# Performance work log

Hardware: AMD Instinct MI355X
Metric: run time of the kernel (lower is better)

## Reference

```python
import jax, jax.numpy as jnp
import numpy as np

B, T = 2, 5            # num_frames MUST equal 5 (Embedding(5, channel) pos table)
C, CTX_C, DH = 384, 128, 64   # channel, context_channel, dim_head (lucidrains default, heads=1)
HW = [(80, 80), (40, 40), (20, 20), (10, 10)]
NS = 4
SCALE = DH ** -0.5


def _xavier(k, shape):
    fan_out, fan_in = shape[-2], shape[-1]
    lim = (6.0 / (fan_in + fan_out)) ** 0.5
    return jax.random.uniform(k, shape, jnp.float32, -lim, lim)


def setup_inputs() -> dict:
    key = jax.random.key(0)
    ks = iter(jax.random.split(key, 40))
    inp = {}
    for i, (h, w) in enumerate(HW):
        inp[f"fmap{i}"] = jax.random.normal(next(ks), (B * T, C, h, w), jnp.float32)
        inp[f"pos{i}"] = jax.random.normal(next(ks), (B, T, C, h, w), jnp.float32)
        inp[f"audio{i}"] = jax.random.normal(next(ks), (B * T, CTX_C), jnp.float32)
    inp["ctx_proj_w"] = _xavier(next(ks), (NS, C, CTX_C))
    inp["ctx_proj_b"] = jnp.zeros((NS, C), jnp.float32)
    inp["pos_emb"] = jax.random.normal(next(ks), (NS, 5, C), jnp.float32)  # Embedding(5, channel) per stage
    inp["qk_w"] = _xavier(next(ks), (NS, DH, C))
    inp["ctx_qk_w"] = _xavier(next(ks), (NS, DH, C))
    inp["v_w"] = _xavier(next(ks), (NS, DH, C))
    inp["ctx_v_w"] = _xavier(next(ks), (NS, DH, C))
    inp["out_w"] = _xavier(next(ks), (NS, C, DH))
    inp["out_b"] = jnp.zeros((NS, C), jnp.float32)
    inp["ctx_out_w"] = _xavier(next(ks), (NS, C, DH))
    inp["ctx_out_b"] = jnp.zeros((NS, C), jnp.float32)
    inp["batch_size"] = B
    inp["num_frames"] = T
    return inp


def _stage(x, pos, audio, Wp, bp, pe, Wqk, Wcqk, Wv, Wcv, Wo, bo, Wco, bco, batch_size):
    bt, c, h, w = x.shape
    # audio projection 128 -> 384
    a = audio @ Wp.T + bp                                  # (bt, C)
    # 'hw' reshape: tokens = H*W per (batch*frame)
    xf = x.reshape(bt, c, h * w).transpose(0, 2, 1)        # (bt, hw, C)
    vp = pos.reshape(bt, c, h * w).transpose(0, 2, 1)      # (bt, hw, C)
    ctx = a[:, None, :]                                    # (bt, 1, C)
    cp = jnp.tile(pe, (batch_size, 1))[:, None, :]         # (bt, 1, C); bt == 5*batch_size
    # bidirectional cross-attention (heads=1), pos added to QK inputs only
    qk = (xf + vp) @ Wqk.T                                 # (bt, hw, DH)
    v = xf @ Wv.T                                          # (bt, hw, DH)
    cqk = (ctx + cp) @ Wcqk.T                              # (bt, 1, DH)
    cv = ctx @ Wcv.T                                       # (bt, 1, DH)
    sim = jnp.einsum('bid,bjd->bij', qk, cqk) * SCALE      # (bt, hw, 1) shared similarity
    attn = jax.nn.softmax(sim, axis=-1)                    # video attends over context (j)
    ctx_attn = jax.nn.softmax(sim, axis=-2)                # context attends over video (i)
    out = jnp.einsum('bij,bjd->bid', attn, cv) @ Wo.T + bo         # (bt, hw, C)
    ctx_out = jnp.einsum('bij,bid->bjd', ctx_attn, v) @ Wco.T + bco  # (bt, 1, C)
    vout = out.transpose(0, 2, 1).reshape(bt, c, h, w)
    aout = ctx_out[:, 0, :]                                # (bt, C)
    return vout, aout


def reference(fmap0, fmap1, fmap2, fmap3, audio0, audio1, audio2, audio3,
              pos0, pos1, pos2, pos3,
              ctx_proj_w, ctx_proj_b, pos_emb, qk_w, ctx_qk_w, v_w, ctx_v_w,
              out_w, out_b, ctx_out_w, ctx_out_b, batch_size, num_frames):
    fmaps = (fmap0, fmap1, fmap2, fmap3)
    poss = (pos0, pos1, pos2, pos3)
    audios = (audio0, audio1, audio2, audio3)
    vouts, aouts = [], []
    for i in range(NS):
        vo, ao = _stage(fmaps[i], poss[i], audios[i],
                        ctx_proj_w[i], ctx_proj_b[i], pos_emb[i],
                        qk_w[i], ctx_qk_w[i], v_w[i], ctx_v_w[i],
                        out_w[i], out_b[i], ctx_out_w[i], ctx_out_b[i], batch_size)
        vouts.append(vo)
        aouts.append(ao)
    return tuple(vouts) + tuple(aouts)
```

## Files before the change

### kernel.cpp

```cpp
#include <hip/hip_runtime.h>

#define BT 10
#define CC 384
#define DH 64
#define CTXC 128
#define NS 4
#define SCALE_F 0.125f

#define VOFF0 0
#define VOFF1 24576000
#define VOFF2 30720000
#define VOFF3 32256000
#define AOUT_OFF 32640000

struct Params {
  const float* fmap0; const float* fmap1; const float* fmap2; const float* fmap3;
  const float* pos0;  const float* pos1;  const float* pos2;  const float* pos3;
  const float* audio0;const float* audio1;const float* audio2;const float* audio3;
  const float* ctx_proj_w; const float* ctx_proj_b; const float* pos_emb;
  const float* qk_w; const float* ctx_qk_w; const float* v_w; const float* ctx_v_w;
  const float* out_w; const float* out_b; const float* ctx_out_w; const float* ctx_out_b;
  float* out;
  float* r;
  float* outvec;
  float* xw;
  float* simbuf;
};

__device__ __forceinline__ int hw_of(int s){ return s==0?6400: s==1?1600: s==2?400:100; }
__device__ __forceinline__ int simoff(int s){ return s==0?0: s==1?64000: s==2?80000:84000; }
__device__ __forceinline__ const float* fm_of(const Params& P, int s){ return s==0?P.fmap0: s==1?P.fmap1: s==2?P.fmap2:P.fmap3; }
__device__ __forceinline__ const float* po_of(const Params& P, int s){ return s==0?P.pos0: s==1?P.pos1: s==2?P.pos2:P.pos3; }
__device__ __forceinline__ const float* au_of(const Params& P, int s){ return s==0?P.audio0: s==1?P.audio1: s==2?P.audio2:P.audio3; }

__global__ __launch_bounds__(384) void k_pre(Params P) {
  const int s = blockIdx.x / BT, b = blockIdx.x % BT;
  const int tid = threadIdx.x;
  __shared__ float aud[CTXC], ctxv[CC], ctxpe[CC], cqk[DH], cvv[DH];
  __shared__ float pq[6][DH], pvv[6][DH];
  const float* audio = au_of(P, s);
  if (tid < CTXC) aud[tid] = audio[b*CTXC + tid];
  __syncthreads();
  {
    float acc = P.ctx_proj_b[s*CC + tid];
    const float* wrow = P.ctx_proj_w + (size_t)(s*CC + tid)*CTXC;
    #pragma unroll 16
    for (int k = 0; k < CTXC; ++k) acc += wrow[k]*aud[k];
    ctxv[tid] = acc;
    ctxpe[tid] = acc + P.pos_emb[(s*5 + (b%5))*CC + tid];
  }
  __syncthreads();
  {
    const int g = tid >> 6, oid = tid & 63;
    float q = 0.f, v = 0.f;
    const float* wq = P.ctx_qk_w + (size_t)(s*DH + oid)*CC + g*64;
    const float* wv = P.ctx_v_w  + (size_t)(s*DH + oid)*CC + g*64;
    #pragma unroll 8
    for (int c = 0; c < 64; ++c) { q += wq[c]*ctxpe[g*64+c]; v += wv[c]*ctxv[g*64+c]; }
    pq[g][oid] = q; pvv[g][oid] = v;
  }
  __syncthreads();
  if (tid < DH) {
    float q = 0.f, v = 0.f;
    #pragma unroll
    for (int g2 = 0; g2 < 6; ++g2) { q += pq[g2][tid]; v += pvv[g2][tid]; }
    cqk[tid] = q; cvv[tid] = v;
  }
  __syncthreads();
  {
    float rr = 0.f, ov = P.out_b[s*CC + tid];
    const float* wqk = P.qk_w + (size_t)s*DH*CC + tid;
    const float* wo  = P.out_w + (size_t)(s*CC + tid)*DH;
    #pragma unroll 8
    for (int d = 0; d < DH; ++d) { rr += wqk[(size_t)d*CC]*cqk[d]; ov += wo[d]*cvv[d]; }
    P.r[(s*BT+b)*CC + tid] = rr * SCALE_F;
    P.outvec[(s*BT+b)*CC + tid] = ov;
  }
}

__global__ __launch_bounds__(256) void k_sim(Params P) {
  const int bid = blockIdx.x;
  int s, b, chunk, part, arr, HW;
  if (bid < 2240)      { s=0; int l=bid;      arr=l&1; l>>=1; part=l&15; l>>=4; chunk=l%7; b=l/7; HW=6400; }
  else if (bid < 2880) { s=1; int l=bid-2240; arr=l&1; l>>=1; part=l&15; l>>=4; chunk=l&1; b=l>>1; HW=1600; }
  else if (bid < 3200) { s=2; int l=bid-2880; arr=l&1; l>>=1; part=l&15; b=l>>4; chunk=0; HW=400; }
  else                 { s=3; int l=bid-3200; arr=l&1; l>>=1; part=l&15; b=l>>4; chunk=0; HW=100; }
  const int tid = threadIdx.x;
  const int c0 = part*24;
  const int hw4 = HW >> 2;

  __shared__ float rs[24];
  if (tid < 24) rs[tid] = P.r[(s*BT+b)*CC + c0 + tid];
  __syncthreads();

  const int i4 = chunk*256 + tid;
  if (i4 < hw4) {
    const float* src = arr ? po_of(P, s) : fm_of(P, s);
    const float4* ap = (const float4*)(src + ((size_t)b*CC + c0)*HW) + i4;
    float4 acc = {0.f, 0.f, 0.f, 0.f};
    for (int cb = 0; cb < 24; cb += 8) {
      float4 v[8];
      #pragma unroll
      for (int u = 0; u < 8; ++u) v[u] = ap[(size_t)(cb+u)*hw4];
      #pragma unroll
      for (int u = 0; u < 8; ++u) {
        const float rc = rs[cb+u];
        acc.x += v[u].x*rc; acc.y += v[u].y*rc; acc.z += v[u].z*rc; acc.w += v[u].w*rc;
      }
    }
    float* dst = P.simbuf + simoff(s) + b*HW + i4*4;
    atomicAdd(dst + 0, acc.x);
    atomicAdd(dst + 1, acc.y);
    atomicAdd(dst + 2, acc.z);
    atomicAdd(dst + 3, acc.w);
  }
}

__global__ __launch_bounds__(256) void k_softmax(Params P) {
  const int s = blockIdx.x / BT, b = blockIdx.x % BT;
  const int HW = hw_of(s);
  float* sim = P.simbuf + simoff(s) + b*HW;
  const int tid = threadIdx.x;
  const int wid = tid >> 6, lane = tid & 63;
  __shared__ float red[4], red2[4];

  float m = -1e30f;
  for (int i = tid; i < HW; i += 256) m = fmaxf(m, sim[i]);
  #pragma unroll
  for (int off = 32; off; off >>= 1) m = fmaxf(m, __shfl_down(m, off));
  if (lane == 0) red[wid] = m;
  __syncthreads();
  if (tid == 0) { float mm = red[0]; for (int w2 = 1; w2 < 4; ++w2) mm = fmaxf(mm, red[w2]); red[0] = mm; }
  __syncthreads();
  m = red[0];

  float sum = 0.f;
  for (int i = tid; i < HW; i += 256) { float e = expf(sim[i] - m); sim[i] = e; sum += e; }
  #pragma unroll
  for (int off = 32; off; off >>= 1) sum += __shfl_down(sum, off);
  if (lane == 0) red2[wid] = sum;
  __syncthreads();
  if (tid == 0) { float ss = red2[0]; for (int w2 = 1; w2 < 4; ++w2) ss += red2[w2]; red2[0] = ss; }
  __syncthreads();
  const float invS = 1.f / red2[0];

  for (int i = tid; i < HW; i += 256) sim[i] *= invS;
}

__global__ __launch_bounds__(256) void k_xw(Params P) {
  const int bid = blockIdx.x;
  const int sb = bid / 96, ct = bid % 96;
  const int s = sb / BT, b = sb % BT;
  const int HW = hw_of(s);
  const int wid = threadIdx.x >> 6, lane = threadIdx.x & 63;
  const int c = ct*4 + wid;
  const float* xrow = fm_of(P, s) + ((size_t)(b*CC + c))*HW;
  const float* wrow = P.simbuf + simoff(s) + b*HW;
  float acc = 0.f;
  for (int i0 = lane*4; i0 < HW; i0 += 1024) {
    float4 x4[4], w4[4];
    #pragma unroll
    for (int u = 0; u < 4; ++u) {
      const int idx = i0 + u*256;
      if (idx < HW) { x4[u] = *(const float4*)(xrow + idx); w4[u] = *(const float4*)(wrow + idx); }
    }
    #pragma unroll
    for (int u = 0; u < 4; ++u) {
      const int idx = i0 + u*256;
      if (idx < HW) acc += x4[u].x*w4[u].x + x4[u].y*w4[u].y + x4[u].z*w4[u].z + x4[u].w*w4[u].w;
    }
  }
  #pragma unroll
  for (int off = 32; off; off >>= 1) acc += __shfl_down(acc, off);
  if (lane == 0) P.xw[(s*BT+b)*CC + c] = acc;
}

__global__ __launch_bounds__(384) void k_post(Params P) {
  const int s = blockIdx.x / BT, b = blockIdx.x % BT;
  const int tid = threadIdx.x;
  __shared__ float xws[CC], ctxo[DH], pc[6][DH];
  xws[tid] = P.xw[(s*BT+b)*CC + tid];
  __syncthreads();
  {
    const int g = tid >> 6, oid = tid & 63;
    float a = 0.f;
    const float* wv = P.v_w + (size_t)(s*DH + oid)*CC + g*64;
    #pragma unroll 8
    for (int c = 0; c < 64; ++c) a += wv[c]*xws[g*64+c];
    pc[g][oid] = a;
  }
  __syncthreads();
  if (tid < DH) {
    float a = 0.f;
    #pragma unroll
    for (int g2 = 0; g2 < 6; ++g2) a += pc[g2][tid];
    ctxo[tid] = a;
  }
  __syncthreads();
  float ao = P.ctx_out_b[s*CC + tid];
  const float* wco = P.ctx_out_w + (size_t)(s*CC + tid)*DH;
  #pragma unroll 8
  for (int d = 0; d < DH; ++d) ao += wco[d]*ctxo[d];
  P.out[(size_t)AOUT_OFF + (s*BT+b)*CC + tid] = ao;
}

template<int F4PR, int VOFF, int OVOFF>
__device__ __forceinline__ void fill_one(const Params& P, int idx) {
  const int row = idx / F4PR;
  const float val = P.outvec[OVOFF + row];
  const float4 v4 = {val, val, val, val};
  ((float4*)(P.out + VOFF))[idx] = v4;
}

__global__ __launch_bounds__(256) void k_fill(Params P) {
  const int gid = blockIdx.x * 256 + threadIdx.x;
  if (blockIdx.x < 24000)      fill_one<1600, VOFF0, 0>    (P, gid);
  else if (blockIdx.x < 30000) fill_one< 400, VOFF1, 3840> (P, gid - 24000*256);
  else if (blockIdx.x < 31500) fill_one< 100, VOFF2, 7680> (P, gid - 30000*256);
  else                         fill_one<  25, VOFF3, 11520>(P, gid - 31500*256);
}

extern "C" void kernel_launch(void* const* d_in, const int* in_sizes, int n_in,
                              void* d_out, int out_size, void* d_ws, size_t ws_size,
                              hipStream_t stream) {
  Params P;
  P.fmap0 = (const float*)d_in[0];  P.pos0 = (const float*)d_in[1];  P.audio0 = (const float*)d_in[2];
  P.fmap1 = (const float*)d_in[3];  P.pos1 = (const float*)d_in[4];  P.audio1 = (const float*)d_in[5];
  P.fmap2 = (const float*)d_in[6];  P.pos2 = (const float*)d_in[7];  P.audio2 = (const float*)d_in[8];
  P.fmap3 = (const float*)d_in[9];  P.pos3 = (const float*)d_in[10]; P.audio3 = (const float*)d_in[11];
  P.ctx_proj_w = (const float*)d_in[12]; P.ctx_proj_b = (const float*)d_in[13];
  P.pos_emb = (const float*)d_in[14];
  P.qk_w = (const float*)d_in[15];  P.ctx_qk_w = (const float*)d_in[16];
  P.v_w = (const float*)d_in[17];   P.ctx_v_w = (const float*)d_in[18];
  P.out_w = (const float*)d_in[19]; P.out_b = (const float*)d_in[20];
  P.ctx_out_w = (const float*)d_in[21]; P.ctx_out_b = (const float*)d_in[22];
  P.out = (float*)d_out;

  float* ws = (float*)d_ws;
  P.r      = ws;
  P.outvec = ws + 15360;
  P.xw     = ws + 30720;
  P.simbuf = ws + 46080;

  hipMemsetAsync(P.simbuf, 0, 85000*sizeof(float), stream);
  k_pre    <<<NS*BT, 384, 0, stream>>>(P);
  k_sim    <<<3520,  256, 0, stream>>>(P);
  k_softmax<<<NS*BT, 256, 0, stream>>>(P);
  k_xw     <<<3840,  256, 0, stream>>>(P);
  k_post   <<<NS*BT, 384, 0, stream>>>(P);
  k_fill   <<<31875, 256, 0, stream>>>(P);
}
```

Measured before the change: 441.0 us.

## Replace atomic sim accumulation with partial buffers, vectorize weight loads, coarsen fill

Result: no change. 435.6 us (-1.2%).

```diff
diff --git a/kernel.cpp b/kernel.cpp
--- a/kernel.cpp
+++ b/kernel.cpp
@@ -12,6 +12,9 @@
 #define VOFF2 30720000
 #define VOFF3 32256000
 #define AOUT_OFF 32640000
+
+#define SIM_TOT 85000
+#define NPART 16
 
 struct Params {
   const float* fmap0; const float* fmap1; const float* fmap2; const float* fmap3;
@@ -24,7 +27,8 @@
   float* r;
   float* outvec;
   float* xw;
-  float* simbuf;
+  float* comb;
+  float* part;
 };
 
 __device__ __forceinline__ int hw_of(int s){ return s==0?6400: s==1?1600: s==2?400:100; }
@@ -43,9 +47,12 @@
   __syncthreads();
   {
     float acc = P.ctx_proj_b[s*CC + tid];
-    const float* wrow = P.ctx_proj_w + (size_t)(s*CC + tid)*CTXC;
-    #pragma unroll 16
-    for (int k = 0; k < CTXC; ++k) acc += wrow[k]*aud[k];
+    const float4* wrow = (const float4*)(P.ctx_proj_w + (size_t)(s*CC + tid)*CTXC);
+    #pragma unroll 8
+    for (int k = 0; k < CTXC/4; ++k) {
+      const float4 w = wrow[k];
+      acc += w.x*aud[k*4] + w.y*aud[k*4+1] + w.z*aud[k*4+2] + w.w*aud[k*4+3];
+    }
     ctxv[tid] = acc;
     ctxpe[tid] = acc + P.pos_emb[(s*5 + (b%5))*CC + tid];
   }
@@ -53,10 +60,15 @@
   {
     const int g = tid >> 6, oid = tid & 63;
     float q = 0.f, v = 0.f;
-    const float* wq = P.ctx_qk_w + (size_t)(s*DH + oid)*CC + g*64;
-    const float* wv = P.ctx_v_w  + (size_t)(s*DH + oid)*CC + g*64;
-    #pragma unroll 8
-    for (int c = 0; c < 64; ++c) { q += wq[c]*ctxpe[g*64+c]; v += wv[c]*ctxv[g*64+c]; }
+    const float4* wq = (const float4*)(P.ctx_qk_w + (size_t)(s*DH + oid)*CC + g*64);
+    const float4* wv = (const float4*)(P.ctx_v_w  + (size_t)(s*DH + oid)*CC + g*64);
+    #pragma unroll
+    for (int u = 0; u < 16; ++u) {
+      const float4 a = wq[u], c = wv[u];
+      const int k0 = g*64 + u*4;
+      q += a.x*ctxpe[k0] + a.y*ctxpe[k0+1] + a.z*ctxpe[k0+2] + a.w*ctxpe[k0+3];
+      v += c.x*ctxv[k0]  + c.y*ctxv[k0+1]  + c.z*ctxv[k0+2]  + c.w*ctxv[k0+3];
+    }
     pq[g][oid] = q; pvv[g][oid] = v;
   }
   __syncthreads();
@@ -70,9 +82,14 @@
   {
     float rr = 0.f, ov = P.out_b[s*CC + tid];
     const float* wqk = P.qk_w + (size_t)s*DH*CC + tid;
-    const float* wo  = P.out_w + (size_t)(s*CC + tid)*DH;
+    const float4* wo = (const float4*)(P.out_w + (size_t)(s*CC + tid)*DH);
     #pragma unroll 8
-    for (int d = 0; d < DH; ++d) { rr += wqk[(size_t)d*CC]*cqk[d]; ov += wo[d]*cvv[d]; }
+    for (int d = 0; d < DH; ++d) rr += wqk[(size_t)d*CC]*cqk[d];
+    #pragma unroll
+    for (int u = 0; u < 16; ++u) {
+      const float4 w = wo[u];
+      ov += w.x*cvv[u*4] + w.y*cvv[u*4+1] + w.z*cvv[u*4+2] + w.w*cvv[u*4+3];
+    }
     P.r[(s*BT+b)*CC + tid] = rr * SCALE_F;
     P.outvec[(s*BT+b)*CC + tid] = ov;
   }
@@ -80,11 +97,11 @@
 
 __global__ __launch_bounds__(256) void k_sim(Params P) {
   const int bid = blockIdx.x;
-  int s, b, chunk, part, arr, HW;
-  if (bid < 2240)      { s=0; int l=bid;      arr=l&1; l>>=1; part=l&15; l>>=4; chunk=l%7; b=l/7; HW=6400; }
-  else if (bid < 2880) { s=1; int l=bid-2240; arr=l&1; l>>=1; part=l&15; l>>=4; chunk=l&1; b=l>>1; HW=1600; }
-  else if (bid < 3200) { s=2; int l=bid-2880; arr=l&1; l>>=1; part=l&15; b=l>>4; chunk=0; HW=400; }
-  else                 { s=3; int l=bid-3200; arr=l&1; l>>=1; part=l&15; b=l>>4; chunk=0; HW=100; }
+  int s, b, chunk, part, HW;
+  if (bid < 1120)      { s=0; int l=bid;      part=l&15; l>>=4; chunk=l%7; b=l/7; HW=6400; }
+  else if (bid < 1440) { s=1; int l=bid-1120; part=l&15; l>>=4; chunk=l&1; b=l>>1; HW=1600; }
+  else if (bid < 1600) { s=2; int l=bid-1440; part=l&15; b=l>>4; chunk=0; HW=400; }
+  else                 { s=3; int l=bid-1600; part=l&15; b=l>>4; chunk=0; HW=100; }
   const int tid = threadIdx.x;
   const int c0 = part*24;
   const int hw4 = HW >> 2;
@@ -95,31 +112,51 @@
 
   const int i4 = chunk*256 + tid;
   if (i4 < hw4) {
-    const float* src = arr ? po_of(P, s) : fm_of(P, s);
-    const float4* ap = (const float4*)(src + ((size_t)b*CC + c0)*HW) + i4;
+    const float4* xp = (const float4*)(fm_of(P, s) + ((size_t)b*CC + c0)*HW) + i4;
+    const float4* pp = (const float4*)(po_of(P, s) + ((size_t)b*CC + c0)*HW) + i4;
     float4 acc = {0.f, 0.f, 0.f, 0.f};
+    #pragma unroll
     for (int cb = 0; cb < 24; cb += 8) {
       float4 v[8];
       #pragma unroll
-      for (int u = 0; u < 8; ++u) v[u] = ap[(size_t)(cb+u)*hw4];
+      for (int u = 0; u < 8; ++u) v[u] = xp[(size_t)(cb+u)*hw4];
       #pragma unroll
       for (int u = 0; u < 8; ++u) {
         const float rc = rs[cb+u];
         acc.x += v[u].x*rc; acc.y += v[u].y*rc; acc.z += v[u].z*rc; acc.w += v[u].w*rc;
       }
     }
-    float* dst = P.simbuf + simoff(s) + b*HW + i4*4;
-    atomicAdd(dst + 0, acc.x);
-    atomicAdd(dst + 1, acc.y);
-    atomicAdd(dst + 2, acc.z);
-    atomicAdd(dst + 3, acc.w);
-  }
+    #pragma unroll
+    for (int cb = 0; cb < 24; cb += 8) {
+      float4 v[8];
+      #pragma unroll
+      for (int u = 0; u < 8; ++u) v[u] = pp[(size_t)(cb+u)*hw4];
+      #pragma unroll
+      for (int u = 0; u < 8; ++u) {
+        const float rc = rs[cb+u];
+        acc.x += v[u].x*rc; acc.y += v[u].y*rc; acc.z += v[u].z*rc; acc.w += v[u].w*rc;
+      }
+    }
+    *(float4*)(P.part + (size_t)part*SIM_TOT + simoff(s) + b*HW + i4*4) = acc;
+  }
+}
+
+__global__ __launch_bounds__(256) void k_comb(Params P) {
+  const int idx = blockIdx.x*256 + threadIdx.x;
+  if (idx >= SIM_TOT/4) return;
+  float4 acc = {0.f, 0.f, 0.f, 0.f};
+  #pragma unroll
+  for (int p = 0; p < NPART; ++p) {
+    const float4 v = *(const float4*)(P.part + (size_t)p*SIM_TOT + idx*4);
+    acc.x += v.x; acc.y += v.y; acc.z += v.z; acc.w += v.w;
+  }
+  *(float4*)(P.comb + idx*4) = acc;
 }
 
 __global__ __launch_bounds__(256) void k_softmax(Params P) {
   const int s = blockIdx.x / BT, b = blockIdx.x % BT;
   const int HW = hw_of(s);
-  float* sim = P.simbuf + simoff(s) + b*HW;
+  float* sim = P.comb + simoff(s) + b*HW;
   const int tid = threadIdx.x;
   const int wid = tid >> 6, lane = tid & 63;
   __shared__ float red[4], red2[4];
@@ -155,7 +192,7 @@
   const int wid = threadIdx.x >> 6, lane = threadIdx.x & 63;
   const int c = ct*4 + wid;
   const float* xrow = fm_of(P, s) + ((size_t)(b*CC + c))*HW;
-  const float* wrow = P.simbuf + simoff(s) + b*HW;
+  const float* wrow = P.comb + simoff(s) + b*HW;
   float acc = 0.f;
   for (int i0 = lane*4; i0 < HW; i0 += 1024) {
     float4 x4[4], w4[4];
@@ -184,9 +221,13 @@
   {
     const int g = tid >> 6, oid = tid & 63;
     float a = 0.f;
-    const float* wv = P.v_w + (size_t)(s*DH + oid)*CC + g*64;
-    #pragma unroll 8
-    for (int c = 0; c < 64; ++c) a += wv[c]*xws[g*64+c];
+    const float4* wv = (const float4*)(P.v_w + (size_t)(s*DH + oid)*CC + g*64);
+    #pragma unroll
+    for (int u = 0; u < 16; ++u) {
+      const float4 w = wv[u];
+      const int k0 = g*64 + u*4;
+      a += w.x*xws[k0] + w.y*xws[k0+1] + w.z*xws[k0+2] + w.w*xws[k0+3];
+    }
     pc[g][oid] = a;
   }
   __syncthreads();
@@ -198,26 +239,35 @@
   }
   __syncthreads();
   float ao = P.ctx_out_b[s*CC + tid];
-  const float* wco = P.ctx_out_w + (size_t)(s*CC + tid)*DH;
-  #pragma unroll 8
-  for (int d = 0; d < DH; ++d) ao += wco[d]*ctxo[d];
+  const float4* wco = (const float4*)(P.ctx_out_w + (size_t)(s*CC + tid)*DH);
+  #pragma unroll
+  for (int u = 0; u < 16; ++u) {
+    const float4 w = wco[u];
+    ao += w.x*ctxo[u*4] + w.y*ctxo[u*4+1] + w.z*ctxo[u*4+2] + w.w*ctxo[u*4+3];
+  }
   P.out[(size_t)AOUT_OFF + (s*BT+b)*CC + tid] = ao;
 }
 
-template<int F4PR, int VOFF, int OVOFF>
-__device__ __forceinline__ void fill_one(const Params& P, int idx) {
-  const int row = idx / F4PR;
-  const float val = P.outvec[OVOFF + row];
-  const float4 v4 = {val, val, val, val};
-  ((float4*)(P.out + VOFF))[idx] = v4;
+template<int F4PR, int VOFF, int OVOFF, int MAXF4>
+__device__ __forceinline__ void fill_one(const Params& P, int lb, int tid) {
+  const int base = lb*1024;
+  #pragma unroll
+  for (int u = 0; u < 4; ++u) {
+    const int idx = base + u*256 + tid;
+    if (MAXF4 % 1024 != 0 && idx >= MAXF4) return;
+    const int row = idx / F4PR;
+    const float val = P.outvec[OVOFF + row];
+    const float4 v4 = {val, val, val, val};
+    ((float4*)(P.out + VOFF))[idx] = v4;
+  }
 }
 
 __global__ __launch_bounds__(256) void k_fill(Params P) {
-  const int gid = blockIdx.x * 256 + threadIdx.x;
-  if (blockIdx.x < 24000)      fill_one<1600, VOFF0, 0>    (P, gid);
-  else if (blockIdx.x < 30000) fill_one< 400, VOFF1, 3840> (P, gid - 24000*256);
-  else if (blockIdx.x < 31500) fill_one< 100, VOFF2, 7680> (P, gid - 30000*256);
-  else                         fill_one<  25, VOFF3, 11520>(P, gid - 31500*256);
+  const int tid = threadIdx.x;
+  if (blockIdx.x < 6000)      fill_one<1600, VOFF0, 0,     6144000>(P, blockIdx.x,        tid);
+  else if (blockIdx.x < 7500) fill_one< 400, VOFF1, 3840,  1536000>(P, blockIdx.x - 6000, tid);
+  else if (blockIdx.x < 7875) fill_one< 100, VOFF2, 7680,   384000>(P, blockIdx.x - 7500, tid);
+  else                        fill_one<  25, VOFF3, 11520,   96000>(P, blockIdx.x - 7875, tid);
 }
 
 extern "C" void kernel_launch(void* const* d_in, const int* in_sizes, int n_in,
@@ -240,13 +290,14 @@
   P.r      = ws;
   P.outvec = ws + 15360;
   P.xw     = ws + 30720;
-  P.simbuf = ws + 46080;
-
-  hipMemsetAsync(P.simbuf, 0, 85000*sizeof(float), stream);
+  P.comb   = ws + 46080;
+  P.part   = ws + 131080;
+
   k_pre    <<<NS*BT, 384, 0, stream>>>(P);
-  k_sim    <<<3520,  256, 0, stream>>>(P);
+  k_sim    <<<1760,  256, 0, stream>>>(P);
+  k_comb   <<<84,    256, 0, stream>>>(P);
   k_softmax<<<NS*BT, 256, 0, stream>>>(P);
   k_xw     <<<3840,  256, 0, stream>>>(P);
   k_post   <<<NS*BT, 384, 0, stream>>>(P);
-  k_fill   <<<31875, 256, 0, stream>>>(P);
-}
+  k_fill   <<<7969,  256, 0, stream>>>(P);
+}
```
